# Optimization experiments

Measured on AMD Instinct MI355X. Metric: run time of the kernel, lower is better.

## Reference

```python
import jax, jax.numpy as jnp
import numpy as np

B, PLEN, D = 32, 1024, 256


def setup_inputs() -> dict:
    key = jax.random.key(0)
    ks = jax.random.split(key, 8)
    u = lambda k, shape: jax.random.uniform(k, shape, jnp.float32, -0.05, 0.05)
    return {
        "P": jax.random.normal(ks[0], (B, PLEN, D), jnp.float32),
        "w_itr_att": u(ks[1], (3 * D,)),
        "w1": u(ks[2], (2 * D, D)),
        "w2": u(ks[3], (2 * D, D)),
        "w3": u(ks[4], (2 * D, D)),
        "b1": u(ks[5], (D,)),
        "b2": u(ks[6], (D,)),
        "b3": u(ks[7], (D,)),
    }


def reference(P, w_itr_att, w1, w2, w3, b1, b2, b3):
    d = P.shape[-1]
    # alpha(a,b) = w_itr_att . [a ; b ; a*b]; split w into the three d-chunks
    wa, wb, wc = w_itr_att[:d], w_itr_att[d:2 * d], w_itr_att[2 * d:]
    # pairwise score A[b,i,j] = wa.P_i + wb.P_j + wc.(P_i * P_j)
    sa = P @ wa                                   # (b, p)
    sb = P @ wb                                   # (b, p)
    A = sa[:, :, None] + sb[:, None, :] + jnp.einsum('bid,bjd->bij', P * wc, P)
    itr_attn = jnp.einsum('bij,bjd->bid', jax.nn.softmax(A, axis=2), P)
    cat = jnp.concatenate([P, itr_attn], axis=-1)  # (b, p, 2d)
    z = jnp.tanh(cat @ w1 + b1)
    r = jax.nn.sigmoid(cat @ w2 + b2)
    f = jax.nn.sigmoid(cat @ w3 + b3)
    return r * P + f * z
```

## Files before the change

### kernel.cpp

```cpp
#include <hip/hip_runtime.h>
#include <hip/hip_bf16.h>

typedef unsigned short u16;
typedef unsigned int   u32;

using bf16x8 = __attribute__((ext_vector_type(8))) short;
using f32x4  = __attribute__((ext_vector_type(4))) float;

#define NB 32
#define NP 1024
#define ND 256

__device__ __forceinline__ u16 f2bf(float x){
  u32 u = __float_as_uint(x);
  u += 0x7FFFu + ((u >> 16) & 1u);
  return (u16)(u >> 16);
}

__device__ __forceinline__ float bf2f(u16 x){
  return __uint_as_float((u32)x << 16);
}

__device__ __forceinline__ void glds16(const void* g, void* l){
  __builtin_amdgcn_global_load_lds((const __attribute__((address_space(1))) void*)g,
                                   (__attribute__((address_space(3))) void*)l, 16, 0, 0);
}

__global__ void prep_pt(const float* __restrict__ P, const float* __restrict__ wi,
                        u16* __restrict__ Pbf, u16* __restrict__ PbfT,
                        float* __restrict__ sbv){
  const int b = blockIdx.y, jt = blockIdx.x;
  __shared__ __align__(16) u16 T[64][264];
  const int tid = threadIdx.x;
  const int row = tid >> 2;
  const int dq  = tid & 3;
  const size_t grow = (size_t)b * NP + jt * 64 + row;
  const float* prow = P + grow * ND;
  const float* wbp  = wi + ND;
  float s = 0.f;
  #pragma unroll
  for (int it = 0; it < 4; ++it){
    const int d0 = it * 64 + dq * 16;
    float4 a0 = *(const float4*)(prow + d0);
    float4 a1 = *(const float4*)(prow + d0 + 4);
    float4 a2 = *(const float4*)(prow + d0 + 8);
    float4 a3 = *(const float4*)(prow + d0 + 12);
    float4 w0 = *(const float4*)(wbp + d0);
    float4 w1 = *(const float4*)(wbp + d0 + 4);
    float4 w2 = *(const float4*)(wbp + d0 + 8);
    float4 w3 = *(const float4*)(wbp + d0 + 12);
    s += a0.x*w0.x + a0.y*w0.y + a0.z*w0.z + a0.w*w0.w;
    s += a1.x*w1.x + a1.y*w1.y + a1.z*w1.z + a1.w*w1.w;
    s += a2.x*w2.x + a2.y*w2.y + a2.z*w2.z + a2.w*w2.w;
    s += a3.x*w3.x + a3.y*w3.y + a3.z*w3.z + a3.w*w3.w;
    u16 tmp[16];
    tmp[0]=f2bf(a0.x); tmp[1]=f2bf(a0.y); tmp[2]=f2bf(a0.z); tmp[3]=f2bf(a0.w);
    tmp[4]=f2bf(a1.x); tmp[5]=f2bf(a1.y); tmp[6]=f2bf(a1.z); tmp[7]=f2bf(a1.w);
    tmp[8]=f2bf(a2.x); tmp[9]=f2bf(a2.y); tmp[10]=f2bf(a2.z); tmp[11]=f2bf(a2.w);
    tmp[12]=f2bf(a3.x); tmp[13]=f2bf(a3.y); tmp[14]=f2bf(a3.z); tmp[15]=f2bf(a3.w);
    *(uint4*)&T[row][d0]     = *(uint4*)tmp;
    *(uint4*)&T[row][d0 + 8] = *(uint4*)(tmp + 8);
    *(uint4*)(Pbf + grow * ND + d0)     = *(uint4*)tmp;
    *(uint4*)(Pbf + grow * ND + d0 + 8) = *(uint4*)(tmp + 8);
  }
  s += __shfl_xor(s, 1, 64);
  s += __shfl_xor(s, 2, 64);
  if (dq == 0) sbv[grow] = s;
  __syncthreads();
  #pragma unroll
  for (int it = 0; it < 8; ++it){
    int cc = tid + 256 * it;
    int d = cc >> 3, c8 = cc & 7;
    u16 tmp[8];
    #pragma unroll
    for (int k = 0; k < 8; ++k) tmp[k] = T[c8 * 8 + k][d];
    *(uint4*)(PbfT + ((size_t)b * ND + d) * NP + jt * 64 + c8 * 8) = *(uint4*)tmp;
  }
}

__global__ void prep_w(const float* __restrict__ w1, const float* __restrict__ w2,
                       const float* __restrict__ w3, u16* __restrict__ Wp){
  const int t = blockIdx.x;
  const float* w = (t < 16) ? w1 : ((t < 32) ? w2 : w3);
  const int tid = threadIdx.x;
  #pragma unroll
  for (int j = 0; j < 4; ++j){
    int item = tid + 256 * j;
    int c = item >> 6, lane = item & 63;
    int ncol = ((t & 15) << 4) + (lane & 15);
    int k0 = 32 * c + 8 * (lane >> 4);
    u16 tmp[8];
    #pragma unroll
    for (int e = 0; e < 8; ++e) tmp[e] = f2bf(w[(size_t)(k0 + e) * 256 + ncol]);
    *(uint4*)(Wp + ((size_t)(t * 16 + c) * 64 + lane) * 8) = *(uint4*)tmp;
  }
}

__launch_bounds__(256, 2)
__global__ void attn_kernel(const float* __restrict__ P, const float* __restrict__ wi,
                            const u16* __restrict__ Pbf, const u16* __restrict__ PbfT,
                            const float* __restrict__ sbv, u16* __restrict__ attnb){
  const int p    = blockIdx.x;
  const int bid  = ((p & 7) << 6) | (p >> 3);
  const int b    = bid >> 4;
  const int q0   = (bid & 15) << 6;
  const int tid  = threadIdx.x;
  const int wave = tid >> 6, lane = tid & 63, lo = lane & 15, hi = lane >> 4;

  __shared__ __align__(16) u16 KtA[64 * 256];
  __shared__ __align__(16) u16 VtA[256 * 64];
  __shared__ __align__(16) u16 Sp[4][16][72];
  __shared__ float sls[4][16];
  __shared__ float lfin[64];
  __shared__ u32 fastf[4];
  char* KtB = (char*)KtA;
  char* VtB = (char*)VtA;

  bf16x8 qf[8];
  {
    const int qrow = q0 + wave * 16 + lo;
    const float* prow = P  + ((size_t)b * NP + qrow) * ND;
    const float* wcp  = wi + 512;
    #pragma unroll
    for (int c = 0; c < 8; ++c){
      const int d0 = 32 * c + 8 * hi;
      float4 a  = *(const float4*)(prow + d0);
      float4 a2 = *(const float4*)(prow + d0 + 4);
      float4 wa  = *(const float4*)(wcp + d0);
      float4 wa2 = *(const float4*)(wcp + d0 + 4);
      bf16x8 q;
      q[0]=(short)f2bf(a.x*wa.x);  q[1]=(short)f2bf(a.y*wa.y);
      q[2]=(short)f2bf(a.z*wa.z);  q[3]=(short)f2bf(a.w*wa.w);
      q[4]=(short)f2bf(a2.x*wa2.x); q[5]=(short)f2bf(a2.y*wa2.y);
      q[6]=(short)f2bf(a2.z*wa2.z); q[7]=(short)f2bf(a2.w*wa2.w);
      qf[c] = q;
    }
  }

  f32x4 of[4][4];
  #pragma unroll
  for (int qt = 0; qt < 4; ++qt)
    #pragma unroll
    for (int dt = 0; dt < 4; ++dt) of[qt][dt] = (f32x4){0.f,0.f,0.f,0.f};
  float mx[4] = {-1e30f,-1e30f,-1e30f,-1e30f};
  float ls[4] = {0.f,0.f,0.f,0.f};

  const u16* kslab = Pbf  + (size_t)b * NP * ND;
  const u16* vslab = PbfT + (size_t)b * ND * NP;

  auto stageK = [&](int kt){
    const int kbase = kt * 64;
    #pragma unroll
    for (int it = 0; it < 8; ++it){
      int off = it * 4096 + tid * 16;
      int j   = off >> 9;
      int ck  = ((off >> 4) & 31) ^ (j & 7);
      glds16((const char*)(kslab + (size_t)(kbase + j) * ND + ck * 8), KtB + off);
    }
  };
  auto stageV = [&](int kt){
    const int kbase = kt * 64;
    #pragma unroll
    for (int it = 0; it < 8; ++it){
      int off = it * 4096 + tid * 16;
      int d   = off >> 7;
      int kc  = ((off >> 4) & 7) ^ (d & 7);
      glds16((const char*)(vslab + (size_t)d * NP + kbase + kc * 8), VtB + off);
    }
  };

  float sbc[4], sbn[4];
  stageK(0);
  stageV(0);
  #pragma unroll
  for (int nt = 0; nt < 4; ++nt) sbc[nt] = sbv[(size_t)b * NP + nt * 16 + lo];
  __syncthreads();

  for (int kt = 0; kt < 16; ++kt){
    f32x4 s[4];
    #pragma unroll
    for (int nt = 0; nt < 4; ++nt){
      f32x4 acc = (f32x4){0.f,0.f,0.f,0.f};
      #pragma unroll
      for (int c = 0; c < 8; ++c){
        int j  = nt * 16 + lo;
        int ad = j * 512 + (((4 * c + hi) ^ (j & 7)) << 4);
        bf16x8 kf = *(const bf16x8*)(KtB + ad);
        acc = __builtin_amdgcn_mfma_f32_16x16x32_bf16(qf[c], kf, acc, 0, 0, 0);
      }
      s[nt] = acc;
      float sv = sbc[nt];
      #pragma unroll
      for (int r = 0; r < 4; ++r) s[nt][r] += sv;
    }

    float scale[4] = {1.f, 1.f, 1.f, 1.f};
    int fast = 1;
    {
      float md = -1e30f;
      #pragma unroll
      for (int nt = 0; nt < 4; ++nt)
        #pragma unroll
        for (int r = 0; r < 4; ++r) md = fmaxf(md, s[nt][r] - mx[r]);
      if (!__all(md <= 8.f)){
        fast = 0;
        #pragma unroll
        for (int r = 0; r < 4; ++r){
          float v = fmaxf(fmaxf(s[0][r], s[1][r]), fmaxf(s[2][r], s[3][r]));
          v = fmaxf(v, __shfl_xor(v, 1, 64));
          v = fmaxf(v, __shfl_xor(v, 2, 64));
          v = fmaxf(v, __shfl_xor(v, 4, 64));
          v = fmaxf(v, __shfl_xor(v, 8, 64));
          float mnew = fmaxf(mx[r], v);
          scale[r] = __expf(mx[r] - mnew);
          mx[r] = mnew;
          ls[r] *= scale[r];
        }
      }
    }
    #pragma unroll
    for (int nt = 0; nt < 4; ++nt)
      #pragma unroll
      for (int r = 0; r < 4; ++r){
        float pv = __expf(s[nt][r] - mx[r]);
        ls[r] += pv;
        Sp[wave][4 * hi + r][16 * nt + lo] = f2bf(pv);
      }
    if (lane == 0) fastf[wave] = (u32)fast;
    if (lo == 0){
      #pragma unroll
      for (int r = 0; r < 4; ++r) sls[wave][4 * hi + r] = scale[r];
    }

    __syncthreads();
    if (kt < 15) stageK(kt + 1);

    if (!(fastf[0] & fastf[1] & fastf[2] & fastf[3])){
      #pragma unroll
      for (int qt = 0; qt < 4; ++qt){
        #pragma unroll
        for (int r = 0; r < 4; ++r){
          float sc = sls[qt][4 * hi + r];
          #pragma unroll
          for (int dt = 0; dt < 4; ++dt) of[qt][dt][r] *= sc;
        }
      }
    }

    #pragma unroll
    for (int kk = 0; kk < 2; ++kk){
      bf16x8 pa[4];
      #pragma unroll
      for (int qt = 0; qt < 4; ++qt)
        pa[qt] = *(const bf16x8*)&Sp[qt][lo][32 * kk + 8 * hi];
      #pragma unroll
      for (int dt = 0; dt < 4; ++dt){
        int d  = wave * 64 + dt * 16 + lo;
        int ad = d * 128 + (((4 * kk + hi) ^ (d & 7)) << 4);
        bf16x8 vb = *(const bf16x8*)(VtB + ad);
        #pragma unroll
        for (int qt = 0; qt < 4; ++qt)
          of[qt][dt] = __builtin_amdgcn_mfma_f32_16x16x32_bf16(pa[qt], vb, of[qt][dt], 0, 0, 0);
      }
    }

    __syncthreads();
    if (kt < 15){
      stageV(kt + 1);
      #pragma unroll
      for (int nt = 0; nt < 4; ++nt)
        sbn[nt] = sbv[(size_t)b * NP + (kt + 1) * 64 + nt * 16 + lo];
      sbc[0] = sbn[0]; sbc[1] = sbn[1]; sbc[2] = sbn[2]; sbc[3] = sbn[3];
    }
  }

  #pragma unroll
  for (int r = 0; r < 4; ++r){
    ls[r] += __shfl_xor(ls[r], 1, 64);
    ls[r] += __shfl_xor(ls[r], 2, 64);
    ls[r] += __shfl_xor(ls[r], 4, 64);
    ls[r] += __shfl_xor(ls[r], 8, 64);
  }
  if (lo == 0){
    #pragma unroll
    for (int r = 0; r < 4; ++r) lfin[wave * 16 + 4 * hi + r] = ls[r];
  }
  __syncthreads();
  #pragma unroll
  for (int qt = 0; qt < 4; ++qt){
    #pragma unroll
    for (int r = 0; r < 4; ++r){
      const float inv = 1.f / lfin[qt * 16 + 4 * hi + r];
      const int qrow = q0 + qt * 16 + 4 * hi + r;
      #pragma unroll
      for (int dt = 0; dt < 4; ++dt){
        float o = of[qt][dt][r] * inv;
        attnb[((size_t)b * NP + qrow) * ND + wave * 64 + dt * 16 + lo] = f2bf(o);
      }
    }
  }
}

__launch_bounds__(256, 2)
__global__ void mlp_kernel(const u16* __restrict__ Pbf, const u16* __restrict__ attnb,
                           const u16* __restrict__ Wp,
                           const float* __restrict__ b1, const float* __restrict__ b2,
                           const float* __restrict__ b3, float* __restrict__ out){
  const int p    = blockIdx.x;
  const int swz  = ((p & 7) << 7) | (p >> 3);
  const int mt   = swz >> 2, cg = swz & 3;
  const int tid  = threadIdx.x;
  const int wave = tid >> 6, lane = tid & 63, lo = lane & 15, hi = lane >> 4;
  const int tq   = 4 * cg + wave;
  const int m0   = mt * 128;

  __shared__ __align__(16) u16 Ab[2][128 * 64];

  f32x4 acc[3][8];
  #pragma unroll
  for (int e = 0; e < 3; ++e)
    #pragma unroll
    for (int m = 0; m < 8; ++m) acc[e][m] = (f32x4){0.f,0.f,0.f,0.f};

  auto stage = [&](int s, int buf){
    const u16* xs = (s < 4) ? (Pbf   + (size_t)m0 * ND + s * 64)
                            : (attnb + (size_t)m0 * ND + (s - 4) * 64);
    char* dst = (char*)Ab[buf];
    #pragma unroll
    for (int it = 0; it < 4; ++it){
      int off = it * 4096 + wave * 1024 + lane * 16;
      int row = off >> 7;
      int cl  = (off & 127) ^ ((row & 7) << 4);
      glds16((const char*)(xs + (size_t)row * ND) + cl, dst + it * 4096 + wave * 1024);
    }
  };

  stage(0, 0);
  __syncthreads();

  for (int s = 0; s < 8; ++s){
    if (s < 7) stage(s + 1, (s + 1) & 1);
    const char* ab = (const char*)Ab[s & 1];
    #pragma unroll
    for (int cc = 0; cc < 2; ++cc){
      const int c = 2 * s + cc;
      bf16x8 wf[3];
      #pragma unroll
      for (int e = 0; e < 3; ++e)
        wf[e] = *(const bf16x8*)(Wp + ((size_t)((tq + 16 * e) * 16 + c) * 64 + lane) * 8);
      #pragma unroll
      for (int m = 0; m < 8; ++m){
        int row = 16 * m + lo;
        bf16x8 af = *(const bf16x8*)(ab + row * 128 + ((64 * cc + 16 * hi) ^ ((row & 7) << 4)));
        #pragma unroll
        for (int e = 0; e < 3; ++e)
          acc[e][m] = __builtin_amdgcn_mfma_f32_16x16x32_bf16(af, wf[e], acc[e][m], 0, 0, 0);
      }
    }
    __syncthreads();
  }

  const int d = 16 * tq + lo;
  const float bb1 = b1[d], bb2 = b2[d], bb3 = b3[d];
  #pragma unroll
  for (int m = 0; m < 8; ++m){
    #pragma unroll
    for (int r = 0; r < 4; ++r){
      const int row = m0 + 16 * m + 4 * hi + r;
      float y1 = acc[0][m][r] + bb1;
      float y2 = acc[1][m][r] + bb2;
      float y3 = acc[2][m][r] + bb3;
      float pv = bf2f(Pbf[(size_t)row * ND + d]);
      float e2 = __expf(2.f * y1);
      float z  = (e2 - 1.f) / (e2 + 1.f);
      float rr = 1.f / (1.f + __expf(-y2));
      float ff = 1.f / (1.f + __expf(-y3));
      out[(size_t)row * ND + d] = rr * pv + ff * z;
    }
  }
}

extern "C" void kernel_launch(void* const* d_in, const int* in_sizes, int n_in,
                              void* d_out, int out_size, void* d_ws, size_t ws_size,
                              hipStream_t stream){
  const float* P  = (const float*)d_in[0];
  const float* wi = (const float*)d_in[1];
  const float* w1 = (const float*)d_in[2];
  const float* w2 = (const float*)d_in[3];
  const float* w3 = (const float*)d_in[4];
  const float* b1 = (const float*)d_in[5];
  const float* b2 = (const float*)d_in[6];
  const float* b3 = (const float*)d_in[7];
  float* out = (float*)d_out;

  char* ws = (char*)d_ws;
  u16*   Pbf   = (u16*)  (ws);
  u16*   PbfT  = (u16*)  (ws + (16u << 20));
  u16*   attnb = (u16*)  (ws + (32u << 20));
  u16*   Wp    = (u16*)  (ws + (48u << 20));
  float* sbv   = (float*)(ws + (49u << 20));

  prep_pt<<<dim3(16, 32), 256, 0, stream>>>(P, wi, Pbf, PbfT, sbv);
  prep_w<<<48, 256, 0, stream>>>(w1, w2, w3, Wp);
  attn_kernel<<<512, 256, 0, stream>>>(P, wi, Pbf, PbfT, sbv, attnb);
  mlp_kernel<<<1024, 256, 0, stream>>>(Pbf, attnb, Wp, b1, b2, b3, out);
}
```

Measured before the change: 109.0 us.

## Compute attention scores QK^T with FP8 MFMA instead of BF16

Adds an FP8 (e4m3) copy of P in the prep kernel and switches the score GEMM in the attention kernel to 16x16x32 fp8 MFMA. The query operand is prescaled by 16 and the accumulator rescaled by 1/16 to keep products out of the FP8 subnormal range. K tiles in LDS shrink to half size and half as many global-to-LDS loads are needed. The cost is lower precision in the softmax logits and an extra output written by the prep kernel.

```diff
diff --git a/kernel.cpp b/kernel.cpp
--- a/kernel.cpp
+++ b/kernel.cpp
@@ -3,6 +3,7 @@
 
 typedef unsigned short u16;
 typedef unsigned int   u32;
+typedef unsigned char  u8;
 
 using bf16x8 = __attribute__((ext_vector_type(8))) short;
 using f32x4  = __attribute__((ext_vector_type(4))) float;
@@ -21,6 +22,36 @@
   return __uint_as_float((u32)x << 16);
 }
 
+#if __has_builtin(__builtin_amdgcn_cvt_pk_fp8_f32)
+template<bool HI>
+__device__ __forceinline__ u32 pk_fp8(float a, float b, u32 old){
+  return (u32)__builtin_amdgcn_cvt_pk_fp8_f32(a, b, (int)old, HI);
+}
+#else
+__device__ __forceinline__ u8 f2e4m3(float x){
+  u32 b = __float_as_uint(x);
+  u32 s = (b >> 31) << 7;
+  float ax = __uint_as_float(b & 0x7fffffffu);
+  if (!(ax < 464.f)) return (u8)(s | 0x7E);
+  if (ax < 0.001953125f) return (u8)s;
+  if (ax < 0.015625f){
+    u32 m = (u32)__float2int_rn(ax * 512.f);
+    return (u8)(s | m);
+  }
+  u32 bb = b & 0x7fffffffu;
+  bb += 0x7ffffu + ((bb >> 20) & 1u);
+  int e = (int)(bb >> 23) - 127 + 7;
+  u32 m = (bb >> 20) & 7u;
+  if (e > 15 || (e == 15 && m == 7)) return (u8)(s | 0x7E);
+  return (u8)(s | ((u32)e << 3) | m);
+}
+template<bool HI>
+__device__ __forceinline__ u32 pk_fp8(float a, float b, u32 old){
+  u32 v = (u32)f2e4m3(a) | ((u32)f2e4m3(b) << 8);
+  return HI ? ((old & 0xFFFFu) | (v << 16)) : ((old & 0xFFFF0000u) | v);
+}
+#endif
+
 __device__ __forceinline__ void glds16(const void* g, void* l){
   __builtin_amdgcn_global_load_lds((const __attribute__((address_space(1))) void*)g,
                                    (__attribute__((address_space(3))) void*)l, 16, 0, 0);
@@ -28,7 +59,7 @@
 
 __global__ void prep_pt(const float* __restrict__ P, const float* __restrict__ wi,
                         u16* __restrict__ Pbf, u16* __restrict__ PbfT,
-                        float* __restrict__ sbv){
+                        u8* __restrict__ P8, float* __restrict__ sbv){
   const int b = blockIdx.y, jt = blockIdx.x;
   __shared__ __align__(16) u16 T[64][264];
   const int tid = threadIdx.x;
@@ -62,6 +93,12 @@
     *(uint4*)&T[row][d0 + 8] = *(uint4*)(tmp + 8);
     *(uint4*)(Pbf + grow * ND + d0)     = *(uint4*)tmp;
     *(uint4*)(Pbf + grow * ND + d0 + 8) = *(uint4*)(tmp + 8);
+    u32 q0 = pk_fp8<false>(a0.x, a0.y, 0); q0 = pk_fp8<true>(a0.z, a0.w, q0);
+    u32 q1 = pk_fp8<false>(a1.x, a1.y, 0); q1 = pk_fp8<true>(a1.z, a1.w, q1);
+    u32 q2 = pk_fp8<false>(a2.x, a2.y, 0); q2 = pk_fp8<true>(a2.z, a2.w, q2);
+    u32 q3 = pk_fp8<false>(a3.x, a3.y, 0); q3 = pk_fp8<true>(a3.z, a3.w, q3);
+    uint4 pq; pq.x = q0; pq.y = q1; pq.z = q2; pq.w = q3;
+    *(uint4*)(P8 + grow * ND + d0) = pq;
   }
   s += __shfl_xor(s, 1, 64);
   s += __shfl_xor(s, 2, 64);
@@ -98,7 +135,7 @@
 
 __launch_bounds__(256, 2)
 __global__ void attn_kernel(const float* __restrict__ P, const float* __restrict__ wi,
-                            const u16* __restrict__ Pbf, const u16* __restrict__ PbfT,
+                            const u8* __restrict__ P8, const u16* __restrict__ PbfT,
                             const float* __restrict__ sbv, u16* __restrict__ attnb){
   const int p    = blockIdx.x;
   const int bid  = ((p & 7) << 6) | (p >> 3);
@@ -107,16 +144,16 @@
   const int tid  = threadIdx.x;
   const int wave = tid >> 6, lane = tid & 63, lo = lane & 15, hi = lane >> 4;
 
-  __shared__ __align__(16) u16 KtA[64 * 256];
+  __shared__ __align__(16) u8  Kt8[64 * 256];
   __shared__ __align__(16) u16 VtA[256 * 64];
   __shared__ __align__(16) u16 Sp[4][16][72];
   __shared__ float sls[4][16];
   __shared__ float lfin[64];
   __shared__ u32 fastf[4];
-  char* KtB = (char*)KtA;
+  char* KtB = (char*)Kt8;
   char* VtB = (char*)VtA;
 
-  bf16x8 qf[8];
+  long qf8[8];
   {
     const int qrow = q0 + wave * 16 + lo;
     const float* prow = P  + ((size_t)b * NP + qrow) * ND;
@@ -128,12 +165,11 @@
       float4 a2 = *(const float4*)(prow + d0 + 4);
       float4 wa  = *(const float4*)(wcp + d0);
       float4 wa2 = *(const float4*)(wcp + d0 + 4);
-      bf16x8 q;
-      q[0]=(short)f2bf(a.x*wa.x);  q[1]=(short)f2bf(a.y*wa.y);
-      q[2]=(short)f2bf(a.z*wa.z);  q[3]=(short)f2bf(a.w*wa.w);
-      q[4]=(short)f2bf(a2.x*wa2.x); q[5]=(short)f2bf(a2.y*wa2.y);
-      q[6]=(short)f2bf(a2.z*wa2.z); q[7]=(short)f2bf(a2.w*wa2.w);
-      qf[c] = q;
+      u32 w0 = pk_fp8<false>(16.f*a.x*wa.x,  16.f*a.y*wa.y,  0);
+      w0     = pk_fp8<true >(16.f*a.z*wa.z,  16.f*a.w*wa.w,  w0);
+      u32 w1 = pk_fp8<false>(16.f*a2.x*wa2.x, 16.f*a2.y*wa2.y, 0);
+      w1     = pk_fp8<true >(16.f*a2.z*wa2.z, 16.f*a2.w*wa2.w, w1);
+      qf8[c] = (long)(((unsigned long long)w1 << 32) | w0);
     }
   }
 
@@ -145,17 +181,17 @@
   float mx[4] = {-1e30f,-1e30f,-1e30f,-1e30f};
   float ls[4] = {0.f,0.f,0.f,0.f};
 
-  const u16* kslab = Pbf  + (size_t)b * NP * ND;
+  const u8*  kslab = P8   + (size_t)b * NP * ND;
   const u16* vslab = PbfT + (size_t)b * ND * NP;
 
   auto stageK = [&](int kt){
     const int kbase = kt * 64;
     #pragma unroll
-    for (int it = 0; it < 8; ++it){
+    for (int it = 0; it < 4; ++it){
       int off = it * 4096 + tid * 16;
-      int j   = off >> 9;
-      int ck  = ((off >> 4) & 31) ^ (j & 7);
-      glds16((const char*)(kslab + (size_t)(kbase + j) * ND + ck * 8), KtB + off);
+      int j   = off >> 8;
+      int u   = ((off >> 4) & 15) ^ (j & 7);
+      glds16((const char*)(kslab + (size_t)(kbase + j) * ND + u * 16), KtB + off);
     }
   };
   auto stageV = [&](int kt){
@@ -184,14 +220,13 @@
       #pragma unroll
       for (int c = 0; c < 8; ++c){
         int j  = nt * 16 + lo;
-        int ad = j * 512 + (((4 * c + hi) ^ (j & 7)) << 4);
-        bf16x8 kf = *(const bf16x8*)(KtB + ad);
-        acc = __builtin_amdgcn_mfma_f32_16x16x32_bf16(qf[c], kf, acc, 0, 0, 0);
-      }
-      s[nt] = acc;
+        int ad = j * 256 + (((2 * c + (hi >> 1)) ^ (j & 7)) << 4) + 8 * (hi & 1);
+        long kf8 = *(const long*)(KtB + ad);
+        acc = __builtin_amdgcn_mfma_f32_16x16x32_fp8_fp8(qf8[c], kf8, acc, 0, 0, 0);
+      }
       float sv = sbc[nt];
       #pragma unroll
-      for (int r = 0; r < 4; ++r) s[nt][r] += sv;
+      for (int r = 0; r < 4; ++r) s[nt][r] = fmaf(acc[r], 0.0625f, sv);
     }
 
     float scale[4] = {1.f, 1.f, 1.f, 1.f};
@@ -399,9 +434,10 @@
   u16*   attnb = (u16*)  (ws + (32u << 20));
   u16*   Wp    = (u16*)  (ws + (48u << 20));
   float* sbv   = (float*)(ws + (49u << 20));
-
-  prep_pt<<<dim3(16, 32), 256, 0, stream>>>(P, wi, Pbf, PbfT, sbv);
+  u8*    P8    = (u8*)   (ws + (50u << 20));
+
+  prep_pt<<<dim3(16, 32), 256, 0, stream>>>(P, wi, Pbf, PbfT, P8, sbv);
   prep_w<<<48, 256, 0, stream>>>(w1, w2, w3, Wp);
-  attn_kernel<<<512, 256, 0, stream>>>(P, wi, Pbf, PbfT, sbv, attnb);
+  attn_kernel<<<512, 256, 0, stream>>>(P, wi, P8, PbfT, sbv, attnb);
   mlp_kernel<<<1024, 256, 0, stream>>>(Pbf, attnb, Wp, b1, b2, b3, out);
 }
```

Result: no change. 108.0 us (-0.9%).
